# Kernel tuning notes

Hardware: AMD Instinct MI355X
Metric: run time of the kernel (lower is better)

## Reference

```python
import jax, jax.numpy as jnp
import numpy as np

EPS = 1e-8  # RMSNormMultiHead default eps (forward passes self.eps)


def rms_norm_multihead(x, weight):
    # x: (B, L, H, d); normalize over last dim in float32, then scale per (H, d)
    x32 = x.astype(jnp.float32)
    normed = x32 * jax.lax.rsqrt(jnp.mean(x32 * x32, axis=-1, keepdims=True) + EPS)
    return normed.astype(x.dtype) * weight


def setup_inputs() -> dict:
    key = jax.random.key(0)
    k0, k1, k2 = jax.random.split(key, 3)
    B, L, D, H = 2, 1024, 1024, 16
    d = D // H
    X = jax.random.normal(k0, (B, L, D), dtype=jnp.float32)
    Wq = jax.random.normal(k1, (D, D), dtype=jnp.float32) * 0.02  # q_proj weight (out, in)
    Wv = jax.random.normal(k2, (D, D), dtype=jnp.float32) * 0.02  # v_proj weight (out, in)
    q_norm_w = jnp.ones((H, d), dtype=jnp.float32)
    v_norm_w = jnp.ones((H, d), dtype=jnp.float32)
    return {"X": X, "Wq": Wq, "Wv": Wv, "q_norm_w": q_norm_w, "v_norm_w": v_norm_w}


def reference(X, Wq, Wv, q_norm_w, v_norm_w):
    B, L, D = X.shape
    H, d = q_norm_w.shape
    K = X.reshape(B, L, H, d)
    Q = rms_norm_multihead((X @ Wq.T).reshape(B, L, H, d), q_norm_w)
    V = rms_norm_multihead((X @ Wv.T).reshape(B, L, H, d), v_norm_w)
    # cumulative outer-product KV state: (B, L, H, d, e)
    W = jnp.cumsum(jnp.einsum('blhd,blhe->blhde', K, V), axis=1)
    out = jnp.einsum('blhd,blhde->blhe', Q, W).reshape(B, L, D)
    return out
```

## Files before the change

kernel.cpp:

```cpp
#include <hip/hip_runtime.h>

#define BB 2
#define LL 1024
#define DD 1024
#define HH 16
#define NC 16
#define EPSF 1e-8f

typedef __attribute__((ext_vector_type(8))) short bf16x8;
typedef __attribute__((ext_vector_type(4))) float f32x4;
typedef unsigned short u16;

static __device__ inline u16 f2bf(float f) {
    unsigned int u = __builtin_bit_cast(unsigned int, f);
    u += 0x7fff + ((u >> 16) & 1);
    return (u16)(u >> 16);
}

static __device__ inline void gload_lds16(const u16* g, u16* l) {
    __builtin_amdgcn_global_load_lds((const __attribute__((address_space(1))) void*)g,
                                     (__attribute__((address_space(3))) void*)l, 16, 0, 0);
}

__global__ __launch_bounds__(256) void cvt_k(const float* __restrict__ X,
                                             const float* __restrict__ Wq,
                                             const float* __restrict__ Wv,
                                             u16* __restrict__ Xb,
                                             u16* __restrict__ Wqb,
                                             u16* __restrict__ Wvb)
{
    int i = (blockIdx.x * 256 + threadIdx.x) * 4;
    const float* s; u16* d; int off;
    if (i < 2*1024*1024)      { s = X;  d = Xb;  off = i; }
    else if (i < 3*1024*1024) { s = Wq; d = Wqb; off = i - 2*1024*1024; }
    else                      { s = Wv; d = Wvb; off = i - 3*1024*1024; }
    float4 v = *(const float4*)(s + off);
    ushort4 o;
    o.x = f2bf(v.x); o.y = f2bf(v.y); o.z = f2bf(v.z); o.w = f2bf(v.w);
    *(ushort4*)(d + off) = o;
}

__global__ __launch_bounds__(256) void gemm_fused(const u16* __restrict__ Xb,
                                                  const u16* __restrict__ Wqb,
                                                  const u16* __restrict__ Wvb,
                                                  const float* __restrict__ qw,
                                                  const float* __restrict__ vw,
                                                  u16* __restrict__ Qb,
                                                  u16* __restrict__ Vb)
{
    const int K = DD, N = DD;
    const u16* W = blockIdx.z ? Wvb : Wqb;
    const float* nw = blockIdx.z ? vw : qw;
    u16* Y = blockIdx.z ? Vb : Qb;
    __shared__ u16 As0[128 * 32], As1[128 * 32];
    __shared__ u16 Bs0[64 * 32],  Bs1[64 * 32];

    const int tid = threadIdx.x, w = tid >> 6, lane = tid & 63;
    const int quad = lane >> 4, l16 = lane & 15;
    const int m0 = blockIdx.y * 128, n0 = blockIdx.x * 64;
    const int lrow = lane >> 2, lcol = (lane & 3) * 8;

    const u16* gA0 = Xb + (size_t)(m0 + w*16 + lrow) * K + lcol;
    const u16* gA1 = gA0 + (size_t)64 * K;
    const u16* gB0 = W + (size_t)(n0 + w*16 + lrow) * K + lcol;
    u16* lA0_0 = &As0[(w*16) * 32];      u16* lA0_1 = &As1[(w*16) * 32];
    u16* lA1_0 = &As0[(64 + w*16) * 32]; u16* lA1_1 = &As1[(64 + w*16) * 32];
    u16* lB0_0 = &Bs0[(w*16) * 32];      u16* lB0_1 = &Bs1[(w*16) * 32];

    f32x4 acc[2][4] = {};
    for (int k0 = 0; k0 < K; k0 += 64) {
        gload_lds16(gA0 + k0,      lA0_0);
        gload_lds16(gA0 + k0 + 32, lA0_1);
        gload_lds16(gA1 + k0,      lA1_0);
        gload_lds16(gA1 + k0 + 32, lA1_1);
        gload_lds16(gB0 + k0,      lB0_0);
        gload_lds16(gB0 + k0 + 32, lB0_1);
        __syncthreads();
        #pragma unroll
        for (int hh = 0; hh < 2; ++hh) {
            const u16* Ah = hh ? As1 : As0;
            const u16* Bh = hh ? Bs1 : Bs0;
            bf16x8 af[2], bfr[4];
            #pragma unroll
            for (int i = 0; i < 2; ++i)
                af[i] = *(const bf16x8*)&Ah[(w*32 + i*16 + l16) * 32 + quad*8];
            #pragma unroll
            for (int j = 0; j < 4; ++j)
                bfr[j] = *(const bf16x8*)&Bh[(j*16 + l16) * 32 + quad*8];
            #pragma unroll
            for (int i = 0; i < 2; ++i)
                #pragma unroll
                for (int j = 0; j < 4; ++j)
                    acc[i][j] = __builtin_amdgcn_mfma_f32_16x16x32_bf16(af[i], bfr[j], acc[i][j], 0, 0, 0);
        }
        __syncthreads();
    }

    float wv4[4];
    #pragma unroll
    for (int j = 0; j < 4; ++j) wv4[j] = nw[n0 + j*16 + l16];
    #pragma unroll
    for (int i = 0; i < 2; ++i) {
        float ss[4];
        #pragma unroll
        for (int r = 0; r < 4; ++r) {
            float s = 0.f;
            #pragma unroll
            for (int j = 0; j < 4; ++j) s += acc[i][j][r] * acc[i][j][r];
            ss[r] = s;
        }
        #pragma unroll
        for (int off = 1; off < 16; off <<= 1)
            #pragma unroll
            for (int r = 0; r < 4; ++r) ss[r] += __shfl_xor(ss[r], off, 64);
        float sc[4];
        #pragma unroll
        for (int r = 0; r < 4; ++r) sc[r] = rsqrtf(ss[r] * (1.f/64.f) + EPSF);
        #pragma unroll
        for (int r = 0; r < 4; ++r) {
            u16* yp = Y + (size_t)(m0 + w*32 + i*16 + quad*4 + r) * N + n0;
            #pragma unroll
            for (int j = 0; j < 4; ++j)
                yp[j*16 + l16] = f2bf(acc[i][j][r] * sc[r] * wv4[j]);
        }
    }
}

__global__ __launch_bounds__(256) void out_mega(const u16* __restrict__ Xb,
                                                const u16* __restrict__ Qb,
                                                const u16* __restrict__ Vb,
                                                float* __restrict__ out)
{
    const int c = 15 - (blockIdx.x & 15);
    const int bh = blockIdx.x >> 4;
    const int h = bh & 15, b = bh >> 4;
    __shared__ u16 Qs[64][72];
    __shared__ u16 Ko[64][72];
    __shared__ u16 Vo[64][72];
    __shared__ u16 St[64][72];
    __shared__ u16 Kt[64][72];
    __shared__ u16 Vt[64][72];
    const int tid = threadIdx.x;
    const int row = tid >> 2, q = tid & 3;
    const int w = tid >> 6, lane = tid & 63, quad = lane >> 4, l16 = lane & 15;

    {
        size_t gbase = (size_t)(b*LL + c*64 + row) * DD + h*64 + q*16;
        u16 vv[16];
        #pragma unroll
        for (int i = 0; i < 16; i += 4) {
            *(ushort4*)&Qs[row][q*16 + i] = *(const ushort4*)(Qb + gbase + i);
            *(ushort4*)&Ko[row][q*16 + i] = *(const ushort4*)(Xb + gbase + i);
            *(ushort4*)&vv[i] = *(const ushort4*)(Vb + gbase + i);
        }
        #pragma unroll
        for (int i = 0; i < 16; ++i)
            Vo[q*16 + i][row] = vv[i];
    }

    const int we = (w & 1) * 32, wd = (w >> 1) * 32;
    f32x4 sacc[2][2] = {};
    const u16* gK = Xb + (size_t)(b*LL + row) * DD + h*64 + q*16;
    const u16* gV = Vb + (size_t)(b*LL + row) * DD + h*64 + q*16;
    ushort4 kr[4], vr[4];
    if (c > 0) {
        #pragma unroll
        for (int i = 0; i < 4; ++i) {
            kr[i] = *(const ushort4*)(gK + i*4);
            vr[i] = *(const ushort4*)(gV + i*4);
        }
    }
    __syncthreads();
    for (int cp = 0; cp < c; ++cp) {
        #pragma unroll
        for (int i = 0; i < 16; ++i) {
            Kt[q*16 + i][row] = ((const u16*)kr)[i];
            Vt[q*16 + i][row] = ((const u16*)vr)[i];
        }
        __syncthreads();
        if (cp + 1 < c) {
            const u16* nK = gK + (size_t)(cp+1)*64*DD;
            const u16* nV = gV + (size_t)(cp+1)*64*DD;
            #pragma unroll
            for (int i = 0; i < 4; ++i) {
                kr[i] = *(const ushort4*)(nK + i*4);
                vr[i] = *(const ushort4*)(nV + i*4);
            }
        }
        #pragma unroll
        for (int k0 = 0; k0 < 64; k0 += 32) {
            bf16x8 av[2], bv[2];
            #pragma unroll
            for (int i = 0; i < 2; ++i)
                av[i] = *(const bf16x8*)&Vt[we + i*16 + l16][k0 + quad*8];
            #pragma unroll
            for (int j = 0; j < 2; ++j)
                bv[j] = *(const bf16x8*)&Kt[wd + j*16 + l16][k0 + quad*8];
            #pragma unroll
            for (int i = 0; i < 2; ++i)
                #pragma unroll
                for (int j = 0; j < 2; ++j)
                    sacc[i][j] = __builtin_amdgcn_mfma_f32_16x16x32_bf16(av[i], bv[j], sacc[i][j], 0, 0, 0);
        }
        __syncthreads();
    }

    #pragma unroll
    for (int i = 0; i < 2; ++i)
        #pragma unroll
        for (int j = 0; j < 2; ++j)
            #pragma unroll
            for (int r = 0; r < 4; ++r)
                St[we + i*16 + quad*4 + r][wd + j*16 + l16] = f2bf(sacc[i][j][r]);

    const int mo = (w & 1) * 32, no = (w >> 1) * 32;
    f32x4 pacc[2][2] = {};
    #pragma unroll
    for (int k0 = 0; k0 < 64; k0 += 32) {
        bf16x8 aq[2], bk[2];
        #pragma unroll
        for (int i = 0; i < 2; ++i)
            aq[i] = *(const bf16x8*)&Qs[mo + i*16 + l16][k0 + quad*8];
        #pragma unroll
        for (int j = 0; j < 2; ++j)
            bk[j] = *(const bf16x8*)&Ko[no + j*16 + l16][k0 + quad*8];
        #pragma unroll
        for (int i = 0; i < 2; ++i)
            #pragma unroll
            for (int j = 0; j < 2; ++j)
                pacc[i][j] = __builtin_amdgcn_mfma_f32_16x16x32_bf16(aq[i], bk[j], pacc[i][j], 0, 0, 0);
    }
    __syncthreads();
    #pragma unroll
    for (int i = 0; i < 2; ++i)
        #pragma unroll
        for (int j = 0; j < 2; ++j)
            #pragma unroll
            for (int r = 0; r < 4; ++r) {
                int l  = mo + i*16 + quad*4 + r;
                int lp = no + j*16 + l16;
                Ko[l][lp] = (lp <= l) ? f2bf(pacc[i][j][r]) : (u16)0;
            }
    __syncthreads();

    f32x4 acc[2][2] = {};
    #pragma unroll
    for (int k0 = 0; k0 < 64; k0 += 32) {
        bf16x8 a1[2], b1[2], a2[2], b2[2];
        #pragma unroll
        for (int i = 0; i < 2; ++i) {
            a1[i] = *(const bf16x8*)&Ko[mo + i*16 + l16][k0 + quad*8];
            a2[i] = *(const bf16x8*)&Qs[mo + i*16 + l16][k0 + quad*8];
        }
        #pragma unroll
        for (int j = 0; j < 2; ++j) {
            b1[j] = *(const bf16x8*)&Vo[no + j*16 + l16][k0 + quad*8];
            b2[j] = *(const bf16x8*)&St[no + j*16 + l16][k0 + quad*8];
        }
        #pragma unroll
        for (int i = 0; i < 2; ++i)
            #pragma unroll
            for (int j = 0; j < 2; ++j) {
                acc[i][j] = __builtin_amdgcn_mfma_f32_16x16x32_bf16(a1[i], b1[j], acc[i][j], 0, 0, 0);
                acc[i][j] = __builtin_amdgcn_mfma_f32_16x16x32_bf16(a2[i], b2[j], acc[i][j], 0, 0, 0);
            }
    }
    float* op = out + (size_t)(b*LL + c*64) * DD + h*64;
    #pragma unroll
    for (int i = 0; i < 2; ++i)
        #pragma unroll
        for (int j = 0; j < 2; ++j)
            #pragma unroll
            for (int r = 0; r < 4; ++r)
                op[(size_t)(mo + i*16 + quad*4 + r) * DD + no + j*16 + l16] = acc[i][j][r];
}

extern "C" void kernel_launch(void* const* d_in, const int* in_sizes, int n_in,
                              void* d_out, int out_size, void* d_ws, size_t ws_size,
                              hipStream_t stream) {
    const float* X  = (const float*)d_in[0];
    const float* Wq = (const float*)d_in[1];
    const float* Wv = (const float*)d_in[2];
    const float* qw = (const float*)d_in[3];
    const float* vw = (const float*)d_in[4];
    float* out = (float*)d_out;

    u16* Xb  = (u16*)d_ws;
    u16* Wqb = Xb  + (size_t)2*1024*1024;
    u16* Wvb = Wqb + (size_t)1024*1024;
    u16* Qb  = Wvb + (size_t)1024*1024;
    u16* Vb  = Qb  + (size_t)2*1024*1024;

    cvt_k<<<4096, 256, 0, stream>>>(X, Wq, Wv, Xb, Wqb, Wvb);
    gemm_fused<<<dim3(16, 16, 2), 256, 0, stream>>>(Xb, Wqb, Wvb, qw, vw, Qb, Vb);
    out_mega<<<BB*HH*NC, 256, 0, stream>>>(Xb, Qb, Vb, out);
}
```

Baseline: 112.8 us.

## Split chunk KV-state computation into separate kernel and prefix-sum states

Moves the per-chunk K^T V outer-product computation into a new kernel that writes one bf16 64x64 state per chunk to workspace. The output kernel then sums the preceding chunk states from global memory instead of recomputing every earlier chunk's MFMA product serially inside each block. This removes the load imbalance where late chunks redo up to 15 chunk products. In exchange it adds a kernel launch, a global round-trip for the states, and bf16 rounding of each partial state before summation.

```diff
diff --git a/kernel.cpp b/kernel.cpp
--- a/kernel.cpp
+++ b/kernel.cpp
@@ -16,7 +16,10 @@
     u += 0x7fff + ((u >> 16) & 1);
     return (u16)(u >> 16);
 }
-
+static __device__ inline float bf2f(u16 v) {
+    unsigned int u = ((unsigned int)v) << 16;
+    return __builtin_bit_cast(float, u);
+}
 static __device__ inline void gload_lds16(const u16* g, u16* l) {
     __builtin_amdgcn_global_load_lds((const __attribute__((address_space(1))) void*)g,
                                      (__attribute__((address_space(3))) void*)l, 16, 0, 0);
@@ -126,94 +129,117 @@
     }
 }
 
-__global__ __launch_bounds__(256) void out_mega(const u16* __restrict__ Xb,
-                                                const u16* __restrict__ Qb,
+__global__ __launch_bounds__(256) void kv_chunk(const u16* __restrict__ Xb,
                                                 const u16* __restrict__ Vb,
-                                                float* __restrict__ out)
+                                                u16* __restrict__ S)
+{
+    const int c = blockIdx.x & 15, bh = blockIdx.x >> 4;
+    const int h = bh & 15, b = bh >> 4;
+    __shared__ u16 Kt[64][72];
+    __shared__ u16 Vt[64][72];
+    const int tid = threadIdx.x;
+    {
+        const int row = tid >> 2, q = tid & 3;
+        size_t gbase = (size_t)(b*LL + c*64 + row) * DD + h*64 + q*16;
+        u16 kk[16], vv[16];
+        #pragma unroll
+        for (int i = 0; i < 16; i += 4) {
+            *(ushort4*)&kk[i] = *(const ushort4*)(Xb + gbase + i);
+            *(ushort4*)&vv[i] = *(const ushort4*)(Vb + gbase + i);
+        }
+        #pragma unroll
+        for (int i = 0; i < 16; ++i) {
+            Kt[q*16 + i][row] = kk[i];
+            Vt[q*16 + i][row] = vv[i];
+        }
+    }
+    __syncthreads();
+    const int w = tid >> 6, lane = tid & 63, quad = lane >> 4, l16 = lane & 15;
+    const int me = (w & 1) * 32, nd = (w >> 1) * 32;
+    f32x4 acc[2][2] = {};
+    #pragma unroll
+    for (int k0 = 0; k0 < 64; k0 += 32) {
+        bf16x8 av[2], bv[2];
+        #pragma unroll
+        for (int i = 0; i < 2; ++i)
+            av[i] = *(const bf16x8*)&Vt[me + i*16 + l16][k0 + quad*8];
+        #pragma unroll
+        for (int j = 0; j < 2; ++j)
+            bv[j] = *(const bf16x8*)&Kt[nd + j*16 + l16][k0 + quad*8];
+        #pragma unroll
+        for (int i = 0; i < 2; ++i)
+            #pragma unroll
+            for (int j = 0; j < 2; ++j)
+                acc[i][j] = __builtin_amdgcn_mfma_f32_16x16x32_bf16(av[i], bv[j], acc[i][j], 0, 0, 0);
+    }
+    u16* Sp = S + ((size_t)blockIdx.x << 12) + w*1024;
+    #pragma unroll
+    for (int i = 0; i < 2; ++i)
+        #pragma unroll
+        for (int j = 0; j < 2; ++j)
+            #pragma unroll
+            for (int r = 0; r < 4; ++r)
+                Sp[(i*2 + j)*256 + r*64 + lane] = f2bf(acc[i][j][r]);
+}
+
+__global__ __launch_bounds__(256) void out_k2(const u16* __restrict__ Xb,
+                                              const u16* __restrict__ Qb,
+                                              const u16* __restrict__ Vb,
+                                              const u16* __restrict__ S,
+                                              float* __restrict__ out)
 {
     const int c = 15 - (blockIdx.x & 15);
     const int bh = blockIdx.x >> 4;
     const int h = bh & 15, b = bh >> 4;
     __shared__ u16 Qs[64][72];
-    __shared__ u16 Ko[64][72];
-    __shared__ u16 Vo[64][72];
+    __shared__ u16 Ks[64][72];
+    __shared__ u16 Vt[64][72];
     __shared__ u16 St[64][72];
-    __shared__ u16 Kt[64][72];
-    __shared__ u16 Vt[64][72];
     const int tid = threadIdx.x;
-    const int row = tid >> 2, q = tid & 3;
-    const int w = tid >> 6, lane = tid & 63, quad = lane >> 4, l16 = lane & 15;
-
     {
+        const int row = tid >> 2, q = tid & 3;
         size_t gbase = (size_t)(b*LL + c*64 + row) * DD + h*64 + q*16;
         u16 vv[16];
         #pragma unroll
         for (int i = 0; i < 16; i += 4) {
             *(ushort4*)&Qs[row][q*16 + i] = *(const ushort4*)(Qb + gbase + i);
-            *(ushort4*)&Ko[row][q*16 + i] = *(const ushort4*)(Xb + gbase + i);
+            *(ushort4*)&Ks[row][q*16 + i] = *(const ushort4*)(Xb + gbase + i);
             *(ushort4*)&vv[i] = *(const ushort4*)(Vb + gbase + i);
         }
         #pragma unroll
         for (int i = 0; i < 16; ++i)
-            Vo[q*16 + i][row] = vv[i];
-    }
-
-    const int we = (w & 1) * 32, wd = (w >> 1) * 32;
-    f32x4 sacc[2][2] = {};
-    const u16* gK = Xb + (size_t)(b*LL + row) * DD + h*64 + q*16;
-    const u16* gV = Vb + (size_t)(b*LL + row) * DD + h*64 + q*16;
-    ushort4 kr[4], vr[4];
-    if (c > 0) {
-        #pragma unroll
-        for (int i = 0; i < 4; ++i) {
-            kr[i] = *(const ushort4*)(gK + i*4);
-            vr[i] = *(const ushort4*)(gV + i*4);
+            Vt[q*16 + i][row] = vv[i];
+        float facc[16] = {};
+        const u16* Sbase = S + ((size_t)(bh * NC) << 12);
+        for (int cp = 0; cp < c; ++cp) {
+            const u16* Sc = Sbase + ((size_t)cp << 12);
+            #pragma unroll
+            for (int jj = 0; jj < 4; ++jj) {
+                ushort4 sv = *(const ushort4*)(Sc + tid*4 + jj*1024);
+                facc[jj*4+0] += bf2f(sv.x);
+                facc[jj*4+1] += bf2f(sv.y);
+                facc[jj*4+2] += bf2f(sv.z);
+                facc[jj*4+3] += bf2f(sv.w);
+            }
+        }
+        #pragma unroll
+        for (int jj = 0; jj < 4; ++jj) {
+            int g = tid * 4;
+            int ij = (g >> 8) & 3, r = (g >> 6) & 3, ln = g & 63;
+            int e = (jj & 1)*32 + (ij >> 1)*16 + (ln >> 4)*4 + r;
+            int d = (jj >> 1)*32 + (ij & 1)*16 + (ln & 15);
+            ushort4 o;
+            o.x = f2bf(facc[jj*4+0]);
+            o.y = f2bf(facc[jj*4+1]);
+            o.z = f2bf(facc[jj*4+2]);
+            o.w = f2bf(facc[jj*4+3]);
+            *(ushort4*)&St[e][d] = o;
         }
     }
     __syncthreads();
-    for (int cp = 0; cp < c; ++cp) {
-        #pragma unroll
-        for (int i = 0; i < 16; ++i) {
-            Kt[q*16 + i][row] = ((const u16*)kr)[i];
-            Vt[q*16 + i][row] = ((const u16*)vr)[i];
-        }
-        __syncthreads();
-        if (cp + 1 < c) {
-            const u16* nK = gK + (size_t)(cp+1)*64*DD;
-            const u16* nV = gV + (size_t)(cp+1)*64*DD;
-            #pragma unroll
-            for (int i = 0; i < 4; ++i) {
-                kr[i] = *(const ushort4*)(nK + i*4);
-                vr[i] = *(const ushort4*)(nV + i*4);
-            }
-        }
-        #pragma unroll
-        for (int k0 = 0; k0 < 64; k0 += 32) {
-            bf16x8 av[2], bv[2];
-            #pragma unroll
-            for (int i = 0; i < 2; ++i)
-                av[i] = *(const bf16x8*)&Vt[we + i*16 + l16][k0 + quad*8];
-            #pragma unroll
-            for (int j = 0; j < 2; ++j)
-                bv[j] = *(const bf16x8*)&Kt[wd + j*16 + l16][k0 + quad*8];
-            #pragma unroll
-            for (int i = 0; i < 2; ++i)
-                #pragma unroll
-                for (int j = 0; j < 2; ++j)
-                    sacc[i][j] = __builtin_amdgcn_mfma_f32_16x16x32_bf16(av[i], bv[j], sacc[i][j], 0, 0, 0);
-        }
-        __syncthreads();
-    }
-
-    #pragma unroll
-    for (int i = 0; i < 2; ++i)
-        #pragma unroll
-        for (int j = 0; j < 2; ++j)
-            #pragma unroll
-            for (int r = 0; r < 4; ++r)
-                St[we + i*16 + quad*4 + r][wd + j*16 + l16] = f2bf(sacc[i][j][r]);
-
+    const int w = tid >> 6, lane = tid & 63, quad = lane >> 4, l16 = lane & 15;
     const int mo = (w & 1) * 32, no = (w >> 1) * 32;
+
     f32x4 pacc[2][2] = {};
     #pragma unroll
     for (int k0 = 0; k0 < 64; k0 += 32) {
@@ -223,7 +249,7 @@
             aq[i] = *(const bf16x8*)&Qs[mo + i*16 + l16][k0 + quad*8];
         #pragma unroll
         for (int j = 0; j < 2; ++j)
-            bk[j] = *(const bf16x8*)&Ko[no + j*16 + l16][k0 + quad*8];
+            bk[j] = *(const bf16x8*)&Ks[no + j*16 + l16][k0 + quad*8];
         #pragma unroll
         for (int i = 0; i < 2; ++i)
             #pragma unroll
@@ -239,7 +265,7 @@
             for (int r = 0; r < 4; ++r) {
                 int l  = mo + i*16 + quad*4 + r;
                 int lp = no + j*16 + l16;
-                Ko[l][lp] = (lp <= l) ? f2bf(pacc[i][j][r]) : (u16)0;
+                Ks[l][lp] = (lp <= l) ? f2bf(pacc[i][j][r]) : (u16)0;
             }
     __syncthreads();
 
@@ -249,12 +275,12 @@
         bf16x8 a1[2], b1[2], a2[2], b2[2];
         #pragma unroll
         for (int i = 0; i < 2; ++i) {
-            a1[i] = *(const bf16x8*)&Ko[mo + i*16 + l16][k0 + quad*8];
+            a1[i] = *(const bf16x8*)&Ks[mo + i*16 + l16][k0 + quad*8];
             a2[i] = *(const bf16x8*)&Qs[mo + i*16 + l16][k0 + quad*8];
         }
         #pragma unroll
         for (int j = 0; j < 2; ++j) {
-            b1[j] = *(const bf16x8*)&Vo[no + j*16 + l16][k0 + quad*8];
+            b1[j] = *(const bf16x8*)&Vt[no + j*16 + l16][k0 + quad*8];
             b2[j] = *(const bf16x8*)&St[no + j*16 + l16][k0 + quad*8];
         }
         #pragma unroll
@@ -290,8 +316,10 @@
     u16* Wvb = Wqb + (size_t)1024*1024;
     u16* Qb  = Wvb + (size_t)1024*1024;
     u16* Vb  = Qb  + (size_t)2*1024*1024;
+    u16* S   = Vb  + (size_t)2*1024*1024;
 
     cvt_k<<<4096, 256, 0, stream>>>(X, Wq, Wv, Xb, Wqb, Wvb);
     gemm_fused<<<dim3(16, 16, 2), 256, 0, stream>>>(Xb, Wqb, Wvb, qw, vw, Qb, Vb);
-    out_mega<<<BB*HH*NC, 256, 0, stream>>>(Xb, Qb, Vb, out);
-}
+    kv_chunk<<<BB*HH*NC, 256, 0, stream>>>(Xb, Vb, S);
+    out_k2<<<BB*HH*NC, 256, 0, stream>>>(Xb, Qb, Vb, S, out);
+}
```

After: 101.9 us. 9.6% less time.
